# Kernel tuning notes

Hardware: AMD Instinct MI355X
Metric: run time of the kernel (lower is better)

Reference implementation:

```python
import jax, jax.numpy as jnp
import numpy as np

K = 3          # kernel size
KF = K * K     # kernel field = 9
PAD = 1
STRIDE = 1


def _conv(x, w, b):
    y = jax.lax.conv_general_dilated(
        x, w, (STRIDE, STRIDE), [(PAD, PAD), (PAD, PAD)],
        dimension_numbers=('NCHW', 'OIHW', 'NCHW'))
    return y + b[None, :, None, None]


def _bilinear_gather(x, py, px):
    # x: [B,C,H,W]; py/px: [B,KF,Ho,Wo] float sampling coords (zero-pad outside)
    B, C, H, W = x.shape
    xf = x.reshape(B, C, H * W)
    y0 = jnp.floor(py)
    x0 = jnp.floor(px)

    def corner(yc, xc):
        wy = 1.0 - jnp.abs(py - yc)
        wx = 1.0 - jnp.abs(px - xc)
        valid = (yc >= 0) & (yc <= H - 1) & (xc >= 0) & (xc <= W - 1)
        yi = jnp.clip(yc, 0, H - 1).astype(jnp.int32)
        xi = jnp.clip(xc, 0, W - 1).astype(jnp.int32)
        idx = (yi * W + xi).reshape(B, -1)               # [B, KF*Ho*Wo]
        v = jax.vmap(lambda f, i: f[:, i])(xf, idx)      # [B, C, KF*Ho*Wo]
        wgt = (wy * wx * valid.astype(x.dtype)).reshape(B, 1, -1)
        return v * wgt

    return (corner(y0, x0) + corner(y0, x0 + 1) +
            corner(y0 + 1, x0) + corner(y0 + 1, x0 + 1))  # [B,C,KF*Ho*Wo]


def _deform_conv(x, offset, mask, w, b):
    # modulated deformable conv v2 (mmcv offset layout: [y,x] interleaved per kernel pt)
    B, C, H, W = x.shape
    Ho, Wo = mask.shape[2], mask.shape[3]
    kh, kw = jnp.meshgrid(jnp.arange(K), jnp.arange(K), indexing='ij')
    kh = kh.reshape(-1).astype(x.dtype)   # [KF]
    kw = kw.reshape(-1).astype(x.dtype)
    base_y = (jnp.arange(Ho) * STRIDE - PAD).astype(x.dtype)
    base_x = (jnp.arange(Wo) * STRIDE - PAD).astype(x.dtype)
    off = offset.reshape(B, KF, 2, Ho, Wo)
    py = base_y[None, None, :, None] + kh[None, :, None, None] + off[:, :, 0]
    px = base_x[None, None, None, :] + kw[None, :, None, None] + off[:, :, 1]
    val = _bilinear_gather(x, py, px).reshape(B, C, KF, Ho, Wo)
    val = val * mask[:, None]                             # modulate
    out = jnp.einsum('bckhw,ock->bohw', val, w.reshape(w.shape[0], C, KF))
    return out + b[None, :, None, None]


def setup_inputs() -> dict:
    key = jax.random.key(0)
    k1, k2, k3 = jax.random.split(key, 3)
    B, C, H, W = 8, 64, 128, 128
    x = jax.random.normal(k1, (B, C, H, W), dtype=jnp.float32)
    w_om = jax.random.normal(k2, (3 * KF, C, K, K), dtype=jnp.float32) * 0.02
    b_om = jnp.zeros((3 * KF,), dtype=jnp.float32)
    w_dc = jax.random.normal(k3, (64, C, K, K), dtype=jnp.float32) * 0.05
    b_dc = jnp.zeros((64,), dtype=jnp.float32)
    return {"x": x, "w_om": w_om, "b_om": b_om, "w_dc": w_dc, "b_dc": b_dc}


def reference(x, w_om, b_om, w_dc, b_dc):
    om = _conv(x, w_om, b_om)                 # [B, 3*KF, H, W]
    offset = om[:, :2 * KF]
    mask = 2.0 * jax.nn.sigmoid(om[:, 2 * KF:])
    return _deform_conv(x, offset, mask, w_dc, b_dc)
```

## Files before the change

### kernel.cpp

```cpp
#include <hip/hip_runtime.h>
#include <cmath>

#define IH 128
#define IW 128
#define NB 8
#define OFFS_STRIDE 129

typedef __attribute__((ext_vector_type(8))) short bf16x8;
typedef __attribute__((ext_vector_type(4))) float f32x4;
typedef __attribute__((ext_vector_type(2))) float f32x2;

union U4B8 { uint4 u; bf16x8 h; };

#define OFFM_OFF 0
#define XT_OFF   3538944
#define WTDC_OFF (3538944 + 4194304)
#define WTOM_OFF (3538944 + 4194304 + 18432)

__device__ __forceinline__ unsigned short f32_to_bf16(float f) {
    unsigned int u = __float_as_uint(f);
    u += 0x7fffu + ((u >> 16) & 1u);
    return (unsigned short)(u >> 16);
}

__global__ void transpose_weights(const float* __restrict__ w_dc,
                                  const float* __restrict__ w_om,
                                  unsigned short* __restrict__ wt_dc16,
                                  unsigned short* __restrict__ wt_om16) {
    int idx = blockIdx.x * blockDim.x + threadIdx.x;
    if (idx < 9 * 64 * 64) {
        int k = idx >> 12;
        int o = (idx >> 6) & 63;
        int c = idx & 63;
        wt_dc16[idx] = f32_to_bf16(w_dc[(o * 64 + c) * 9 + k]);
    }
    if (idx < 9 * 32 * 64) {
        int k = idx >> 11;
        int o = (idx >> 6) & 31;
        int c = idx & 63;
        wt_om16[idx] = (o < 27) ? f32_to_bf16(w_om[(o * 64 + c) * 9 + k])
                                : (unsigned short)0;
    }
}

__global__ __launch_bounds__(256) void transpose_x(
        const float* __restrict__ x, unsigned short* __restrict__ xT) {
    __shared__ __align__(16) float t[64][132];
    const int tid = threadIdx.x;
    const int b = blockIdx.x >> 7;
    const int h = blockIdx.x & 127;

#pragma unroll
    for (int j = 0; j < 8; ++j) {
        const int i = (j << 8) + tid;
        const int c = i >> 5;
        const int w4 = i & 31;
        const float4 v = *(const float4*)&x[(((size_t)(b * 64 + c)) << 14) + (h << 7) + (w4 << 2)];
        *(float4*)&t[c][w4 << 2] = v;
    }
    __syncthreads();

#pragma unroll
    for (int j = 0; j < 4; ++j) {
        const int u = (j << 8) + tid;
        const int px = u & 127;
        const int cg = u >> 7;
        unsigned int pk[4];
#pragma unroll
        for (int e = 0; e < 4; ++e) {
            const float lo = t[(cg << 3) + 2 * e][px];
            const float hi = t[(cg << 3) + 2 * e + 1][px];
            asm("v_cvt_pk_bf16_f32 %0, %1, %2" : "=v"(pk[e]) : "v"(lo), "v"(hi));
        }
        *(uint4*)(xT + (((size_t)b << 20) + ((size_t)((h << 7) + px) << 6) + (cg << 3))) =
            make_uint4(pk[0], pk[1], pk[2], pk[3]);
    }
}

__global__ __launch_bounds__(256) void conv_om_mfma(
        const unsigned short* __restrict__ xT,
        const float* __restrict__ b_om,
        const unsigned short* __restrict__ wt_om16,
        float* __restrict__ offm) {
    __shared__ __align__(16) unsigned short win[198 * 72];
    __shared__ __align__(16) unsigned short wks[2][32 * 72];

    const int tid = threadIdx.x;
    const int bid = blockIdx.x;
    const int swz = ((bid & 7) << 8) + (bid >> 3);
    const int b = swz >> 8;
    const int rem = swz & 255;
    const int h = rem >> 1;
    const int w0 = (rem & 1) << 6;
    const int wid = tid >> 6;
    const int lane = tid & 63;
    const int ln15 = lane & 15;
    const int quad = lane >> 4;

    for (int idx = tid; idx < 1584; idx += 256) {
        const int pos = idx >> 3;
        const int part = idx & 7;
        const int r = pos / 66;
        const int xx = pos - r * 66;
        const int y = h + r - 1;
        const int xg = w0 + xx - 1;
        uint4 v = make_uint4(0u, 0u, 0u, 0u);
        if (y >= 0 && y < IH && xg >= 0 && xg < IW)
            v = *(const uint4*)(xT + (((size_t)b << 20) + (((y << 7) + xg) << 6) + (part << 3)));
        *(uint4*)&win[pos * 72 + part * 8] = v;
    }
    {
        const int o = tid >> 3;
        const int part = tid & 7;
        *(uint4*)&wks[0][o * 72 + part * 8] =
            *(const uint4*)(wt_om16 + (o << 6) + (part << 3));
    }
    __syncthreads();

    f32x4 acc[2] = {{0.f, 0.f, 0.f, 0.f}, {0.f, 0.f, 0.f, 0.f}};

    for (int k = 0; k < 9; ++k) {
        const int buf = k & 1;
        if (k < 8) {
            const int o = tid >> 3;
            const int part = tid & 7;
            *(uint4*)&wks[buf ^ 1][o * 72 + part * 8] =
                *(const uint4*)(wt_om16 + ((k + 1) << 11) + (o << 6) + (part << 3));
        }
        const int kh = k / 3;
        const int kw = k - kh * 3;
        const int posb = kh * 66 + wid * 16 + ln15 + kw;
        const unsigned short* wb = wks[buf];
#pragma unroll
        for (int ch = 0; ch < 2; ++ch) {
            const int c = (ch << 5) + (quad << 3);
            U4B8 a, b0, b1;
            a.u  = *(const uint4*)&win[posb * 72 + c];
            b0.u = *(const uint4*)&wb[ln15 * 72 + c];
            b1.u = *(const uint4*)&wb[(16 + ln15) * 72 + c];
            acc[0] = __builtin_amdgcn_mfma_f32_16x16x32_bf16(a.h, b0.h, acc[0], 0, 0, 0);
            acc[1] = __builtin_amdgcn_mfma_f32_16x16x32_bf16(a.h, b1.h, acc[1], 0, 0, 0);
        }
        __syncthreads();
    }

    const int px0 = wid * 16 + quad * 4;
#pragma unroll
    for (int ot = 0; ot < 2; ++ot) {
        const int o = (ot << 4) + ln15;
        if (o >= 27) continue;
        const float bias = b_om[o];
        float4 r;
        r.x = acc[ot][0] + bias;
        r.y = acc[ot][1] + bias;
        r.z = acc[ot][2] + bias;
        r.w = acc[ot][3] + bias;
        if (o >= 18) {
            r.x = 2.0f / (1.0f + __expf(-r.x));
            r.y = 2.0f / (1.0f + __expf(-r.y));
            r.z = 2.0f / (1.0f + __expf(-r.z));
            r.w = 2.0f / (1.0f + __expf(-r.w));
        }
        *(float4*)&offm[(((size_t)(b * 27 + o)) << 14) + (h << 7) + w0 + px0] = r;
    }
}

__device__ __forceinline__ void issue_gather(
        const unsigned short* __restrict__ xb, const float* offs,
        int k, int lpx, int h, int quad, uint4* g, float* cw) {
    const float offy = offs[(k << 1) * OFFS_STRIDE + lpx];
    const float offx = offs[((k << 1) + 1) * OFFS_STRIDE + lpx];
    const float msk  = offs[(18 + k) * OFFS_STRIDE + lpx];
    const int kh = k / 3;
    const int kw = k - kh * 3;
    const float py  = (float)(h + kh - 1) + offy;
    const float pxf = (float)(lpx + kw - 1) + offx;
    const float y0f = floorf(py);
    const float x0f = floorf(pxf);
    const float fy = py - y0f;
    const float fx = pxf - x0f;
    const float wy0 = 1.0f - fy, wx0 = 1.0f - fx;
    const float vy0 = (y0f >= 0.0f && y0f <= 127.0f) ? 1.0f : 0.0f;
    const float vy1 = (y0f >= -1.0f && y0f <= 126.0f) ? 1.0f : 0.0f;
    const float vx0 = (x0f >= 0.0f && x0f <= 127.0f) ? 1.0f : 0.0f;
    const float vx1 = (x0f >= -1.0f && x0f <= 126.0f) ? 1.0f : 0.0f;
    cw[0] = wy0 * wx0 * vy0 * vx0 * msk;
    cw[1] = wy0 * fx  * vy0 * vx1 * msk;
    cw[2] = fy  * wx0 * vy1 * vx0 * msk;
    cw[3] = fy  * fx  * vy1 * vx1 * msk;
    const int y0i = min(max((int)y0f, 0), 127);
    const int y1i = min(max((int)y0f + 1, 0), 127);
    const int x0i = min(max((int)x0f, 0), 127);
    const int x1i = min(max((int)x0f + 1, 0), 127);
    const int cofs = quad << 3;
    const unsigned short* p00 = xb + ((((size_t)((y0i << 7) + x0i)) << 6) + cofs);
    const unsigned short* p01 = xb + ((((size_t)((y0i << 7) + x1i)) << 6) + cofs);
    const unsigned short* p10 = xb + ((((size_t)((y1i << 7) + x0i)) << 6) + cofs);
    const unsigned short* p11 = xb + ((((size_t)((y1i << 7) + x1i)) << 6) + cofs);
    g[0] = *(const uint4*)p00;  g[1] = *(const uint4*)(p00 + 32);
    g[2] = *(const uint4*)p01;  g[3] = *(const uint4*)(p01 + 32);
    g[4] = *(const uint4*)p10;  g[5] = *(const uint4*)(p10 + 32);
    g[6] = *(const uint4*)p11;  g[7] = *(const uint4*)(p11 + 32);
}

__device__ __forceinline__ void pack_frags(const uint4* g, const float* cw,
                                           U4B8& a0, U4B8& a1) {
    f32x2 v2[8];
#pragma unroll
    for (int i = 0; i < 8; ++i) v2[i] = (f32x2){0.f, 0.f};
#pragma unroll
    for (int c = 0; c < 4; ++c) {
        f32x2 w2;
        w2.x = cw[c];
        w2.y = cw[c];
        const uint4 ga = g[2 * c];
        const uint4 gb = g[2 * c + 1];
        const unsigned int u[8] = {ga.x, ga.y, ga.z, ga.w, gb.x, gb.y, gb.z, gb.w};
#pragma unroll
        for (int i = 0; i < 8; ++i) {
            f32x2 x2;
            x2.x = __uint_as_float(u[i] << 16);
            x2.y = __uint_as_float(u[i] & 0xffff0000u);
            asm("v_pk_fma_f32 %0, %1, %2, %0" : "+v"(v2[i]) : "v"(x2), "v"(w2));
        }
    }
    unsigned int pk[8];
#pragma unroll
    for (int i = 0; i < 8; ++i)
        asm("v_cvt_pk_bf16_f32 %0, %1, %2"
            : "=v"(pk[i]) : "v"(v2[i].x), "v"(v2[i].y));
    a0.u = make_uint4(pk[0], pk[1], pk[2], pk[3]);
    a1.u = make_uint4(pk[4], pk[5], pk[6], pk[7]);
}

__global__ __launch_bounds__(512) void deform_mfma(
        const unsigned short* __restrict__ xT,
        const float* __restrict__ b_dc,
        const float* __restrict__ offm,
        const unsigned short* __restrict__ wt_dc16,
        float* __restrict__ out) {
    __shared__ __align__(16) float offs[27 * OFFS_STRIDE];
    __shared__ __align__(16) unsigned short wks[2][64 * 72];

    const int tid = threadIdx.x;
    const int bid = blockIdx.x;
    const int swz = ((bid & 7) << 7) + (bid >> 3);
    const int b = swz >> 7;
    const int h = swz & 127;
    const int wid = tid >> 6;
    const int lane = tid & 63;
    const int ln15 = lane & 15;
    const int quad = lane >> 4;
    const int lpx = (wid << 4) + ln15;

    for (int i = tid; i < 27 * 128; i += 512) {
        const int ch = i >> 7;
        const int px = i & 127;
        offs[ch * OFFS_STRIDE + px] =
            offm[(((size_t)(b * 27 + ch)) << 14) + (h << 7) + px];
    }
    const int so = tid >> 3, sp = tid & 7;
    *(uint4*)&wks[0][so * 72 + sp * 8] =
        *(const uint4*)(wt_dc16 + (so << 6) + (sp << 3));
    __syncthreads();

    const unsigned short* xb = xT + ((size_t)b << 20);

    f32x4 acc[4];
#pragma unroll
    for (int i = 0; i < 4; ++i) acc[i] = (f32x4){0.f, 0.f, 0.f, 0.f};

    uint4 g[2][8];
    float cw[2][4];
    issue_gather(xb, offs, 0, lpx, h, quad, g[0], cw[0]);

#pragma unroll
    for (int k = 0; k < 9; ++k) {
        const int cur = k & 1;
        const int nxt = cur ^ 1;
        if (k < 8) {
            const uint4 wv = *(const uint4*)(wt_dc16 + ((k + 1) << 12) + (so << 6) + (sp << 3));
            issue_gather(xb, offs, k + 1, lpx, h, quad, g[nxt], cw[nxt]);
            *(uint4*)&wks[nxt][so * 72 + sp * 8] = wv;
        }
        U4B8 a0, a1;
        pack_frags(g[cur], cw[cur], a0, a1);
        const unsigned short* wb = wks[cur];
#pragma unroll
        for (int ot = 0; ot < 4; ++ot) {
            U4B8 b0, b1;
            const unsigned short* base = &wb[((ot << 4) + ln15) * 72 + (quad << 3)];
            b0.u = *(const uint4*)base;
            b1.u = *(const uint4*)(base + 32);
            acc[ot] = __builtin_amdgcn_mfma_f32_16x16x32_bf16(a0.h, b0.h, acc[ot], 0, 0, 0);
            acc[ot] = __builtin_amdgcn_mfma_f32_16x16x32_bf16(a1.h, b1.h, acc[ot], 0, 0, 0);
        }
        if (k < 8) {
            asm volatile("s_waitcnt lgkmcnt(0)" ::: "memory");
            __builtin_amdgcn_s_barrier();
            __builtin_amdgcn_sched_barrier(0);
        }
    }

#pragma unroll
    for (int ot = 0; ot < 4; ++ot) {
        const int o = (ot << 4) + ln15;
        const float bias = b_dc[o];
        float4 r;
        r.x = acc[ot][0] + bias;
        r.y = acc[ot][1] + bias;
        r.z = acc[ot][2] + bias;
        r.w = acc[ot][3] + bias;
        *(float4*)&out[(((size_t)(b * 64 + o)) << 14) + (h << 7) + (wid << 4) + (quad << 2)] = r;
    }
}

extern "C" void kernel_launch(void* const* d_in, const int* in_sizes, int n_in,
                              void* d_out, int out_size, void* d_ws, size_t ws_size,
                              hipStream_t stream) {
    const float* x    = (const float*)d_in[0];
    const float* w_om = (const float*)d_in[1];
    const float* b_om = (const float*)d_in[2];
    const float* w_dc = (const float*)d_in[3];
    const float* b_dc = (const float*)d_in[4];
    float* out = (float*)d_out;
    float* ws  = (float*)d_ws;

    float* offm = ws + OFFM_OFF;
    unsigned short* xT      = (unsigned short*)(ws + XT_OFF);
    unsigned short* wt_dc16 = (unsigned short*)(ws + WTDC_OFF);
    unsigned short* wt_om16 = (unsigned short*)(ws + WTOM_OFF);

    transpose_weights<<<144, 256, 0, stream>>>(w_dc, w_om, wt_dc16, wt_om16);
    transpose_x<<<NB * IH, 256, 0, stream>>>(x, xT);
    conv_om_mfma<<<NB * IH * 2, 256, 0, stream>>>(xT, b_om, wt_om16, offm);
    deform_mfma<<<NB * IH, 512, 0, stream>>>(xT, b_dc, offm, wt_dc16, out);
}
```

Measured before the change: 181.0 us.

## Split deform blocks into half-rows and preload all weights into swizzled LDS

The deformable conv kernel now uses 256-thread blocks that each cover half an output row, with twice as many blocks. All nine bf16 weight slices are loaded into LDS once, using an XOR-swizzled layout, which removes the per-tap double-buffered weight copy and the barrier inside the k loop. The aim is to drop intra-loop synchronisation and improve occupancy and scheduling. In exchange, each block uses more LDS (about 72KB), which may cap resident blocks per CU, and the offset and weight loads are duplicated across the two half-row blocks.

```diff
diff --git a/kernel.cpp b/kernel.cpp
--- a/kernel.cpp
+++ b/kernel.cpp
@@ -4,7 +4,6 @@
 #define IH 128
 #define IW 128
 #define NB 8
-#define OFFS_STRIDE 129
 
 typedef __attribute__((ext_vector_type(8))) short bf16x8;
 typedef __attribute__((ext_vector_type(4))) float f32x4;
@@ -167,14 +166,14 @@
 
 __device__ __forceinline__ void issue_gather(
         const unsigned short* __restrict__ xb, const float* offs,
-        int k, int lpx, int h, int quad, uint4* g, float* cw) {
-    const float offy = offs[(k << 1) * OFFS_STRIDE + lpx];
-    const float offx = offs[((k << 1) + 1) * OFFS_STRIDE + lpx];
-    const float msk  = offs[(18 + k) * OFFS_STRIDE + lpx];
+        int k, int lpx, int h, int w0, int quad, uint4* g, float* cw) {
+    const float offy = offs[(k << 1) * 64 + lpx];
+    const float offx = offs[((k << 1) + 1) * 64 + lpx];
+    const float msk  = offs[(18 + k) * 64 + lpx];
     const int kh = k / 3;
     const int kw = k - kh * 3;
     const float py  = (float)(h + kh - 1) + offy;
-    const float pxf = (float)(lpx + kw - 1) + offx;
+    const float pxf = (float)(w0 + lpx + kw - 1) + offx;
     const float y0f = floorf(py);
     const float x0f = floorf(pxf);
     const float fy = py - y0f;
@@ -233,35 +232,40 @@
     a1.u = make_uint4(pk[4], pk[5], pk[6], pk[7]);
 }
 
-__global__ __launch_bounds__(512) void deform_mfma(
+__global__ __launch_bounds__(256, 2) void deform_mfma(
         const unsigned short* __restrict__ xT,
         const float* __restrict__ b_dc,
         const float* __restrict__ offm,
         const unsigned short* __restrict__ wt_dc16,
         float* __restrict__ out) {
-    __shared__ __align__(16) float offs[27 * OFFS_STRIDE];
-    __shared__ __align__(16) unsigned short wks[2][64 * 72];
+    __shared__ float offs[27 * 64];
+    __shared__ __align__(16) unsigned short wksAll[9 * 64 * 64];
 
     const int tid = threadIdx.x;
     const int bid = blockIdx.x;
-    const int swz = ((bid & 7) << 7) + (bid >> 3);
-    const int b = swz >> 7;
-    const int h = swz & 127;
+    const int swz = ((bid & 7) << 8) + (bid >> 3);
+    const int b = swz >> 8;
+    const int rem = swz & 255;
+    const int h = rem >> 1;
+    const int w0 = (rem & 1) << 6;
     const int wid = tid >> 6;
     const int lane = tid & 63;
     const int ln15 = lane & 15;
     const int quad = lane >> 4;
     const int lpx = (wid << 4) + ln15;
 
-    for (int i = tid; i < 27 * 128; i += 512) {
-        const int ch = i >> 7;
-        const int px = i & 127;
-        offs[ch * OFFS_STRIDE + px] =
-            offm[(((size_t)(b * 27 + ch)) << 14) + (h << 7) + px];
-    }
-    const int so = tid >> 3, sp = tid & 7;
-    *(uint4*)&wks[0][so * 72 + sp * 8] =
-        *(const uint4*)(wt_dc16 + (so << 6) + (sp << 3));
+    for (int i = tid; i < 1728; i += 256) {
+        offs[i] = offm[(((size_t)(b * 27 + (i >> 6))) << 14) + (h << 7) + w0 + (i & 63)];
+    }
+    for (int s = tid; s < 9 * 512; s += 256) {
+        const int slice = s >> 9;
+        const int idx = s & 511;
+        const int o = idx >> 3;
+        const int sp = idx & 7;
+        const int col = (sp << 4) ^ ((o & 7) << 4);
+        *(uint4*)&wksAll[(slice << 12) + (o << 6) + (col >> 1)] =
+            *(const uint4*)(wt_dc16 + (slice << 12) + (o << 6) + (sp << 3));
+    }
     __syncthreads();
 
     const unsigned short* xb = xT + ((size_t)b << 20);
@@ -272,33 +276,29 @@
 
     uint4 g[2][8];
     float cw[2][4];
-    issue_gather(xb, offs, 0, lpx, h, quad, g[0], cw[0]);
+    issue_gather(xb, offs, 0, lpx, h, w0, quad, g[0], cw[0]);
 
 #pragma unroll
     for (int k = 0; k < 9; ++k) {
         const int cur = k & 1;
         const int nxt = cur ^ 1;
         if (k < 8) {
-            const uint4 wv = *(const uint4*)(wt_dc16 + ((k + 1) << 12) + (so << 6) + (sp << 3));
-            issue_gather(xb, offs, k + 1, lpx, h, quad, g[nxt], cw[nxt]);
-            *(uint4*)&wks[nxt][so * 72 + sp * 8] = wv;
+            issue_gather(xb, offs, k + 1, lpx, h, w0, quad, g[nxt], cw[nxt]);
         }
         U4B8 a0, a1;
         pack_frags(g[cur], cw[cur], a0, a1);
-        const unsigned short* wb = wks[cur];
+        const unsigned short* wb = &wksAll[k << 12];
 #pragma unroll
         for (int ot = 0; ot < 4; ++ot) {
+            const int row = (ot << 4) + ln15;
+            const int xr = (row & 7) << 4;
+            const int c0 = ((quad << 4) ^ xr) >> 1;
+            const int c1 = ((64 + (quad << 4)) ^ xr) >> 1;
             U4B8 b0, b1;
-            const unsigned short* base = &wb[((ot << 4) + ln15) * 72 + (quad << 3)];
-            b0.u = *(const uint4*)base;
-            b1.u = *(const uint4*)(base + 32);
+            b0.u = *(const uint4*)&wb[(row << 6) + c0];
+            b1.u = *(const uint4*)&wb[(row << 6) + c1];
             acc[ot] = __builtin_amdgcn_mfma_f32_16x16x32_bf16(a0.h, b0.h, acc[ot], 0, 0, 0);
             acc[ot] = __builtin_amdgcn_mfma_f32_16x16x32_bf16(a1.h, b1.h, acc[ot], 0, 0, 0);
-        }
-        if (k < 8) {
-            asm volatile("s_waitcnt lgkmcnt(0)" ::: "memory");
-            __builtin_amdgcn_s_barrier();
-            __builtin_amdgcn_sched_barrier(0);
         }
     }
 
@@ -311,7 +311,7 @@
         r.y = acc[ot][1] + bias;
         r.z = acc[ot][2] + bias;
         r.w = acc[ot][3] + bias;
-        *(float4*)&out[(((size_t)(b * 64 + o)) << 14) + (h << 7) + (wid << 4) + (quad << 2)] = r;
+        *(float4*)&out[(((size_t)(b * 64 + o)) << 14) + (h << 7) + w0 + (wid << 4) + (quad << 2)] = r;
     }
 }
 
@@ -334,5 +334,5 @@
     transpose_weights<<<144, 256, 0, stream>>>(w_dc, w_om, wt_dc16, wt_om16);
     transpose_x<<<NB * IH, 256, 0, stream>>>(x, xT);
     conv_om_mfma<<<NB * IH * 2, 256, 0, stream>>>(xT, b_om, wt_om16, offm);
-    deform_mfma<<<NB * IH, 512, 0, stream>>>(xT, b_dc, offm, wt_dc16, out);
-}
+    deform_mfma<<<NB * IH * 2, 256, 0, stream>>>(xT, b_dc, offm, wt_dc16, out);
+}
```

Result: slower. 194.6 us (+7.5%).
